# Kernel tuning notes

Hardware: AMD Instinct MI355X
Metric: run time of the kernel (lower is better)

## Reference

```python
import jax, jax.numpy as jnp
import numpy as np

N_GAUSS = 4_000_000


def setup_inputs() -> dict:
    key = jax.random.key(0)
    k1, k2, k3, k4 = jax.random.split(key, 4)
    return {
        "positions": jax.random.normal(k1, (N_GAUSS, 3), dtype=jnp.float32),
        "colors": jax.random.uniform(k2, (N_GAUSS, 3), dtype=jnp.float32),
        "opacities": jax.random.uniform(k3, (N_GAUSS,), dtype=jnp.float32),
        "camera_params": jax.random.normal(k4, (4, 4), dtype=jnp.float32),
        "image_size": 1024,
    }


def reference(positions, colors, opacities, camera_params, image_size):
    # camera_params is unused by the original simplified rasterizer.
    S = image_size
    N = positions.shape[0]
    # Pixel coords: ((xy + 1) * S / 2).long(), clamped to [0, S-1].
    pix = jnp.clip(((positions[:, :2] + 1.0) * (S / 2)).astype(jnp.int32), 0, S - 1)
    x, y = pix[:, 0], pix[:, 1]
    flat = y * S + x  # [N] linear pixel index (image[0, :, y, x])

    # The torch loop writes gaussians in order i=0..N-1 with plain assignment,
    # scatter-max of the gaussian index per pixel.
    winner = jnp.full((S * S,), -1, dtype=jnp.int32).at[flat].max(
        jnp.arange(N, dtype=jnp.int32)
    )  # [S*S]
    valid = winner >= 0
    w = jnp.maximum(winner, 0)

    rgb = colors[w] * opacities[w][:, None]          # [S*S, 3]
    rgb = jnp.where(valid[:, None], rgb, 0.0)
    alpha = jnp.where(valid, opacities[w], 0.0)       # [S*S]

    img = jnp.concatenate([rgb, alpha[:, None]], axis=-1)  # [S*S, 4]
    # flat = y*S + x -> reshape to [S, S, 4] (y, x, c), then NCHW.
    return img.reshape(S, S, 4).transpose(2, 0, 1)[None]   # [1, 4, S, S]
```

## Files before the change

kernel.cpp:

```cpp
#include <hip/hip_runtime.h>
#include <hip/hip_bf16.h>

#define S_IMG 1024
#define BORDER_SLOTS 4096
#define NB 512
#define NCHUNK 16

__global__ __launch_bounds__(1024) void gr_scatter(const float4* __restrict__ pos4,
                                                   int* __restrict__ winner,
                                                   int* __restrict__ border_scratch,
                                                   int nquad) {
    __shared__ int lds_border[BORDER_SLOTS];
    #pragma unroll
    for (int t = threadIdx.x; t < BORDER_SLOTS; t += 1024) lds_border[t] = -1;
    __syncthreads();

    int c00 = -1, c10 = -1, c01 = -1, c11 = -1;
    const int stride = gridDim.x * 1024;
    for (int q = blockIdx.x * 1024 + threadIdx.x; q < nquad; q += stride) {
        float4 a = pos4[3 * q + 0];
        float4 b = pos4[3 * q + 1];
        float4 c = pos4[3 * q + 2];
        float xs[4] = {a.x, a.w, b.z, c.y};
        float ys[4] = {a.y, b.x, b.w, c.z};
        int base = 4 * q;
        #pragma unroll
        for (int j = 0; j < 4; ++j) {
            int x = (int)((xs[j] + 1.0f) * 512.0f);
            int y = (int)((ys[j] + 1.0f) * 512.0f);
            x = min(max(x, 0), S_IMG - 1);
            y = min(max(y, 0), S_IMG - 1);
            int i = base + j;
            bool xe = (x == 0) | (x == S_IMG - 1);
            bool ye = (y == 0) | (y == S_IMG - 1);
            if (xe & ye) {
                if (x == 0) { if (y == 0) c00 = i; else c01 = i; }
                else        { if (y == 0) c10 = i; else c11 = i; }
            } else if (xe | ye) {
                int idx;
                if (y == 0)              idx = x;
                else if (y == S_IMG - 1) idx = 1024 + x;
                else if (x == 0)         idx = 2048 + (y - 1);
                else                     idx = 3072 + (y - 1);
                atomicMax(&lds_border[idx], i);
            } else {
                atomicMax(&winner[(y << 10) + x], i);
            }
        }
    }
    #pragma unroll
    for (int off = 32; off; off >>= 1) {
        c00 = max(c00, __shfl_xor(c00, off));
        c10 = max(c10, __shfl_xor(c10, off));
        c01 = max(c01, __shfl_xor(c01, off));
        c11 = max(c11, __shfl_xor(c11, off));
    }
    __syncthreads();
    if ((threadIdx.x & 63) == 0) {
        if (c00 >= 0) atomicMax(&lds_border[1024 + 0 - 1024 + 3070], c00);
    }
    __shared__ int csh[4];
    if (threadIdx.x < 4) csh[threadIdx.x] = -1;
    __syncthreads();
    if ((threadIdx.x & 63) == 0) {
        if (c00 >= 0) atomicMax(&csh[0], c00);
        if (c10 >= 0) atomicMax(&csh[1], c10);
        if (c01 >= 0) atomicMax(&csh[2], c01);
        if (c11 >= 0) atomicMax(&csh[3], c11);
    }
    __syncthreads();
    if (threadIdx.x < 4) {
        int v = csh[threadIdx.x];
        if (v >= 0) {
            const int addr[4] = {0, S_IMG - 1, (S_IMG - 1) * S_IMG, S_IMG * S_IMG - 1};
            atomicMax(&winner[addr[threadIdx.x]], v);
        }
    }
    int4* dst = (int4*)(border_scratch + (size_t)blockIdx.x * BORDER_SLOTS);
    const int4* src = (const int4*)lds_border;
    for (int t = threadIdx.x; t < BORDER_SLOTS / 4; t += 1024) dst[t] = src[t];
}

__global__ __launch_bounds__(256) void gr_border_reduce(const int* __restrict__ border_scratch,
                                                        int* __restrict__ winner) {
    int p = blockIdx.x * 256 + threadIdx.x;
    int b0 = blockIdx.y * (NB / NCHUNK);
    int m = -1;
    #pragma unroll 4
    for (int b = 0; b < NB / NCHUNK; ++b)
        m = max(m, border_scratch[(size_t)(b0 + b) * BORDER_SLOTS + p]);
    if (m < 0) return;
    int x, y;
    if (p < 1024)      { x = p;        y = 0; }
    else if (p < 2048) { x = p - 1024; y = S_IMG - 1; }
    else if (p < 3072) { int r = p - 2048; if (r > 1021) return; x = 0;         y = r + 1; }
    else               { int r = p - 3072; if (r > 1021) return; x = S_IMG - 1; y = r + 1; }
    atomicMax(&winner[y * S_IMG + x], m);
}

__global__ __launch_bounds__(256) void gr_resolve(const int* __restrict__ winner,
                                                  const float* __restrict__ colors,
                                                  const float* __restrict__ opacities,
                                                  float* __restrict__ out) {
    const int SS = S_IMG * S_IMG;
    int t = blockIdx.x * 256 + threadIdx.x;
    if (t >= SS / 4) return;
    int4 w4 = *(const int4*)(winner + 4 * t);
    int ws[4] = {w4.x, w4.y, w4.z, w4.w};
    float r[4], g[4], b[4], al[4];
    #pragma unroll
    for (int j = 0; j < 4; ++j) {
        int w = ws[j];
        float rr = 0.f, gg = 0.f, bb = 0.f, aa = 0.f;
        if (w >= 0) {
            float o = opacities[w];
            rr = colors[3 * w + 0] * o;
            gg = colors[3 * w + 1] * o;
            bb = colors[3 * w + 2] * o;
            aa = o;
        }
        r[j] = rr; g[j] = gg; b[j] = bb; al[j] = aa;
    }
    *(float4*)(out + 0 * SS + 4 * t) = make_float4(r[0], r[1], r[2], r[3]);
    *(float4*)(out + 1 * SS + 4 * t) = make_float4(g[0], g[1], g[2], g[3]);
    *(float4*)(out + 2 * SS + 4 * t) = make_float4(b[0], b[1], b[2], b[3]);
    *(float4*)(out + 3 * SS + 4 * t) = make_float4(al[0], al[1], al[2], al[3]);
}

extern "C" void kernel_launch(void* const* d_in, const int* in_sizes, int n_in,
                              void* d_out, int out_size, void* d_ws, size_t ws_size,
                              hipStream_t stream) {
    const float* positions = (const float*)d_in[0];
    const float* colors    = (const float*)d_in[1];
    const float* opacities = (const float*)d_in[2];
    float* out = (float*)d_out;

    const int n  = in_sizes[0] / 3;
    const int SS = S_IMG * S_IMG;

    int* winner         = (int*)d_ws;
    int* border_scratch = winner + SS;

    hipMemsetAsync(winner, 0xFF, (size_t)SS * sizeof(int), stream);

    gr_scatter<<<NB, 1024, 0, stream>>>((const float4*)positions, winner,
                                        border_scratch, n / 4);

    dim3 grid_br(BORDER_SLOTS / 256, NCHUNK);
    gr_border_reduce<<<grid_br, 256, 0, stream>>>(border_scratch, winner);

    gr_resolve<<<(SS / 4 + 255) / 256, 256, 0, stream>>>(winner, colors, opacities, out);
}
```

Measured before the change: 227.0 us.

## Replace per-pixel resolve with per-gaussian paint pass plus output memset

New measurement: 328.9 us. 1.45x slower.

```diff
diff --git a/kernel.cpp b/kernel.cpp
--- a/kernel.cpp
+++ b/kernel.cpp
@@ -11,8 +11,9 @@
                                                    int* __restrict__ border_scratch,
                                                    int nquad) {
     __shared__ int lds_border[BORDER_SLOTS];
-    #pragma unroll
+    __shared__ int csh[4];
     for (int t = threadIdx.x; t < BORDER_SLOTS; t += 1024) lds_border[t] = -1;
+    if (threadIdx.x < 4) csh[threadIdx.x] = -1;
     __syncthreads();
 
     int c00 = -1, c10 = -1, c01 = -1, c11 = -1;
@@ -55,13 +56,6 @@
         c01 = max(c01, __shfl_xor(c01, off));
         c11 = max(c11, __shfl_xor(c11, off));
     }
-    __syncthreads();
-    if ((threadIdx.x & 63) == 0) {
-        if (c00 >= 0) atomicMax(&lds_border[1024 + 0 - 1024 + 3070], c00);
-    }
-    __shared__ int csh[4];
-    if (threadIdx.x < 4) csh[threadIdx.x] = -1;
-    __syncthreads();
     if ((threadIdx.x & 63) == 0) {
         if (c00 >= 0) atomicMax(&csh[0], c00);
         if (c10 >= 0) atomicMax(&csh[1], c10);
@@ -98,33 +92,45 @@
     atomicMax(&winner[y * S_IMG + x], m);
 }
 
-__global__ __launch_bounds__(256) void gr_resolve(const int* __restrict__ winner,
-                                                  const float* __restrict__ colors,
-                                                  const float* __restrict__ opacities,
-                                                  float* __restrict__ out) {
+__global__ __launch_bounds__(256) void gr_paint(const float4* __restrict__ pos4,
+                                                const int* __restrict__ winner,
+                                                const float* __restrict__ colors,
+                                                const float* __restrict__ opacities,
+                                                float* __restrict__ out,
+                                                int nquad) {
     const int SS = S_IMG * S_IMG;
-    int t = blockIdx.x * 256 + threadIdx.x;
-    if (t >= SS / 4) return;
-    int4 w4 = *(const int4*)(winner + 4 * t);
-    int ws[4] = {w4.x, w4.y, w4.z, w4.w};
-    float r[4], g[4], b[4], al[4];
-    #pragma unroll
-    for (int j = 0; j < 4; ++j) {
-        int w = ws[j];
-        float rr = 0.f, gg = 0.f, bb = 0.f, aa = 0.f;
-        if (w >= 0) {
-            float o = opacities[w];
-            rr = colors[3 * w + 0] * o;
-            gg = colors[3 * w + 1] * o;
-            bb = colors[3 * w + 2] * o;
-            aa = o;
+    const int stride = gridDim.x * 256;
+    for (int q = blockIdx.x * 256 + threadIdx.x; q < nquad; q += stride) {
+        float4 a = pos4[3 * q + 0];
+        float4 b = pos4[3 * q + 1];
+        float4 c = pos4[3 * q + 2];
+        float xs[4] = {a.x, a.w, b.z, c.y};
+        float ys[4] = {a.y, b.x, b.w, c.z};
+        int base = 4 * q;
+        int ps[4];
+        #pragma unroll
+        for (int j = 0; j < 4; ++j) {
+            int x = (int)((xs[j] + 1.0f) * 512.0f);
+            int y = (int)((ys[j] + 1.0f) * 512.0f);
+            x = min(max(x, 0), S_IMG - 1);
+            y = min(max(y, 0), S_IMG - 1);
+            ps[j] = (y << 10) + x;
         }
-        r[j] = rr; g[j] = gg; b[j] = bb; al[j] = aa;
+        int w0 = winner[ps[0]], w1 = winner[ps[1]], w2 = winner[ps[2]], w3 = winner[ps[3]];
+        int wv[4] = {w0, w1, w2, w3};
+        #pragma unroll
+        for (int j = 0; j < 4; ++j) {
+            int i = base + j;
+            if (wv[j] == i) {
+                float o = opacities[i];
+                int p = ps[j];
+                out[0 * SS + p] = colors[3 * i + 0] * o;
+                out[1 * SS + p] = colors[3 * i + 1] * o;
+                out[2 * SS + p] = colors[3 * i + 2] * o;
+                out[3 * SS + p] = o;
+            }
+        }
     }
-    *(float4*)(out + 0 * SS + 4 * t) = make_float4(r[0], r[1], r[2], r[3]);
-    *(float4*)(out + 1 * SS + 4 * t) = make_float4(g[0], g[1], g[2], g[3]);
-    *(float4*)(out + 2 * SS + 4 * t) = make_float4(b[0], b[1], b[2], b[3]);
-    *(float4*)(out + 3 * SS + 4 * t) = make_float4(al[0], al[1], al[2], al[3]);
 }
 
 extern "C" void kernel_launch(void* const* d_in, const int* in_sizes, int n_in,
@@ -142,6 +148,7 @@
     int* border_scratch = winner + SS;
 
     hipMemsetAsync(winner, 0xFF, (size_t)SS * sizeof(int), stream);
+    hipMemsetAsync(out, 0, (size_t)out_size * sizeof(float), stream);
 
     gr_scatter<<<NB, 1024, 0, stream>>>((const float4*)positions, winner,
                                         border_scratch, n / 4);
@@ -149,5 +156,6 @@
     dim3 grid_br(BORDER_SLOTS / 256, NCHUNK);
     gr_border_reduce<<<grid_br, 256, 0, stream>>>(border_scratch, winner);
 
-    gr_resolve<<<(SS / 4 + 255) / 256, 256, 0, stream>>>(winner, colors, opacities, out);
+    gr_paint<<<2048, 256, 0, stream>>>((const float4*)positions, winner,
+                                       colors, opacities, out, n / 4);
 }
```
